# Optimization experiments

Hardware: AMD Instinct MI355X
Metric: run time of the kernel (lower is better)

## Reference

```python
import jax, jax.numpy as jnp
import numpy as np

L, D, H, F = 6, 1024, 8, 2048
B, S, IN = 4, 2048, 128
DK = D // H
EPS = 1e-6


def layer_norm(x, s, b):
    mu = jnp.mean(x, -1, keepdims=True)
    var = jnp.mean((x - mu) ** 2, -1, keepdims=True)
    return (x - mu) * jax.lax.rsqrt(var + EPS) * s + b


def rotate_every_two(x):
    x1 = x[..., ::2]
    x2 = x[..., 1::2]
    return jnp.stack([-x2, x1], axis=-1).reshape(x.shape)


def rotary_tables():
    # torchscale RetNet xpos-style angles: each freq repeated twice (interleaved)
    angle = 1.0 / (10000.0 ** jnp.linspace(0.0, 1.0, DK // 2))
    angle = jnp.repeat(angle, 2)                      # [DK]
    idx = jnp.arange(S, dtype=jnp.float32)[:, None]   # [S,1]
    return jnp.sin(idx * angle), jnp.cos(idx * angle)  # [S,DK] each


def decay_mask():
    # gamma_h = 1 - 2^(-5-h); D[h,n,m] = gamma_h^(n-m) for n>=m else 0,
    # row-normalized by sqrt(row sum) as in torchscale.
    gamma = 1.0 - 2.0 ** (-5.0 - jnp.arange(H, dtype=jnp.float32))  # [H]
    n = jnp.arange(S)
    diff = jnp.clip(n[:, None] - n[None, :], 0)                      # [S,S]
    tril = n[:, None] >= n[None, :]
    m = jnp.where(tril[None], gamma[:, None, None] ** diff[None].astype(jnp.float32), 0.0)
    return m / jnp.sqrt(jnp.sum(m, -1, keepdims=True))               # [H,S,S]


def setup_inputs() -> dict:
    key = jax.random.key(0)
    ks = iter(jax.random.split(key, 24))
    p = lambda shape: jax.random.normal(next(ks), shape, jnp.float32) * 0.02
    return {
        "x": jax.random.normal(next(ks), (B, S, IN), jnp.float32),
        "W_in": p((IN, D)), "b_in": jnp.zeros((D,), jnp.float32),
        "Wq": p((L, D, D)), "Wk": p((L, D, D)), "Wv": p((L, D, D)),
        "Wg": p((L, D, D)), "Wo": p((L, D, D)),
        "gn_g": jnp.ones((L, D), jnp.float32),
        "ln1_s": jnp.ones((L, D), jnp.float32), "ln1_b": jnp.zeros((L, D), jnp.float32),
        "ffn_W1": p((L, D, F)), "ffn_b1": jnp.zeros((L, F), jnp.float32),
        "ffn_W2": p((L, F, D)), "ffn_b2": jnp.zeros((L, D), jnp.float32),
        "ln2_s": jnp.ones((L, D), jnp.float32), "ln2_b": jnp.zeros((L, D), jnp.float32),
        "lnf_s": jnp.ones((D,), jnp.float32), "lnf_b": jnp.zeros((D,), jnp.float32),
        "W_reg": p((D, 1)), "b_reg": jnp.zeros((1,), jnp.float32),
    }


def reference(x, W_in, b_in, Wq, Wk, Wv, Wg, Wo, gn_g, ln1_s, ln1_b,
              ffn_W1, ffn_b1, ffn_W2, ffn_b2, ln2_s, ln2_b, lnf_s, lnf_b,
              W_reg, b_reg):
    sin, cos = rotary_tables()
    dmask = decay_mask()  # [H,S,S]
    h = x @ W_in + b_in   # input_embed
    for l in range(L):
        # --- multi-scale retention (pre-norm) ---
        y = layer_norm(h, ln1_s[l], ln1_b[l])
        q = (y @ Wq[l]).reshape(B, S, H, DK).transpose(0, 2, 1, 3)
        k = (y @ Wk[l]).reshape(B, S, H, DK).transpose(0, 2, 1, 3) * (DK ** -0.5)
        v = (y @ Wv[l]).reshape(B, S, H, DK).transpose(0, 2, 1, 3)
        q = q * cos + rotate_every_two(q) * sin
        k = k * cos + rotate_every_two(k) * sin
        scores = jnp.einsum('bhnd,bhmd->bhnm', q, k)
        ret = scores * dmask[None]
        ret = ret / jnp.clip(jnp.abs(ret).sum(-1, keepdims=True), 1.0, None)
        o = jnp.einsum('bhnm,bhmd->bhnd', ret, v)
        # per-head group (RMS) norm
        o = o * jax.lax.rsqrt(jnp.mean(o * o, -1, keepdims=True) + EPS)
        o = o.transpose(0, 2, 1, 3).reshape(B, S, D) * gn_g[l]
        g = y @ Wg[l]
        h = h + (jax.nn.silu(g) * o) @ Wo[l]
        # --- FFN (pre-norm) ---
        y = layer_norm(h, ln2_s[l], ln2_b[l])
        h = h + jax.nn.gelu(y @ ffn_W1[l] + ffn_b1[l]) @ ffn_W2[l] + ffn_b2[l]
    h = layer_norm(h, lnf_s, lnf_b)
    out = 1.1 * jax.nn.sigmoid(h @ W_reg + b_reg) - 0.05
    return out.squeeze(-1)  # [B,S]
```

## Files before the change

kernel.cpp:

```cpp
#include <hip/hip_runtime.h>

#define L_ 6
#define D_ 1024
#define H_ 8
#define F_ 2048
#define B_ 4
#define S_ 2048
#define IN_ 128
#define DK_ 128
#define BS_ (B_*S_)
#define D2_ 4096

typedef short bf16x8 __attribute__((ext_vector_type(8)));
typedef float f32x4 __attribute__((ext_vector_type(4)));

__device__ inline float b2f(unsigned short u){ union{unsigned int i; float f;} v; v.i = ((unsigned int)u)<<16; return v.f; }
__device__ inline unsigned short f2b(float f){ union{unsigned int i; float f;} v; v.f = f; unsigned int r = v.i + 0x7FFFu + ((v.i>>16)&1u); return (unsigned short)(r>>16); }
__device__ inline unsigned int cvtpk(float lo, float hi){
    unsigned int r; asm("v_cvt_pk_bf16_f32 %0, %1, %2" : "=v"(r) : "v"(lo), "v"(hi)); return r;
}

__device__ inline void gld16(const void* g, void* l) {
    __builtin_amdgcn_global_load_lds((const __attribute__((address_space(1))) unsigned int*)g,
                                     (__attribute__((address_space(3))) unsigned int*)l, 16, 0, 0);
}

#define GBAR() do{ asm volatile("" ::: "memory"); __builtin_amdgcn_s_barrier(); asm volatile("" ::: "memory"); }while(0)

__global__ void f32_to_bf16_k(const float* __restrict__ in, unsigned short* __restrict__ out, int n)
{
    int i = blockIdx.x*256 + threadIdx.x;
    if (i < n) out[i] = f2b(in[i]);
}

__global__ void transpose_w_k(const float* __restrict__ in, unsigned short* __restrict__ out, int R, int C, size_t ostride)
{
    __shared__ float tile[32][33];
    int z = blockIdx.z;
    const float* pi = in + (size_t)z*R*C;
    unsigned short* po = out + (size_t)z*ostride;
    int c0 = blockIdx.x*32, r0 = blockIdx.y*32;
    int tx = threadIdx.x, ty = threadIdx.y;
    #pragma unroll
    for (int i=0;i<4;i++) tile[ty+i*8][tx] = pi[(size_t)(r0+ty+i*8)*C + c0+tx];
    __syncthreads();
    #pragma unroll
    for (int i=0;i<4;i++) po[(size_t)(c0+ty+i*8)*R + r0+tx] = f2b(tile[tx][ty+i*8]);
}

__global__ void transpose_v_k(const unsigned short* __restrict__ vb, unsigned short* __restrict__ vT)
{
    __shared__ unsigned short tile[32][33];
    int z = blockIdx.z;
    int b = z >> 3, hh = z & 7;
    int s0 = blockIdx.x*32, d0 = blockIdx.y*32;
    int tx = threadIdx.x, ty = threadIdx.y;
    #pragma unroll
    for (int i=0;i<4;i++) tile[ty+i*8][tx] = vb[(size_t)(b*S_ + s0+ty+i*8)*D2_ + hh*DK_ + d0+tx];
    __syncthreads();
    #pragma unroll
    for (int i=0;i<4;i++) vT[((size_t)z*DK_ + d0+ty+i*8)*S_ + s0+tx] = tile[tx][ty+i*8];
}

__global__ void build_sincos_k(float* __restrict__ cost, float* __restrict__ sint)
{
    int id = blockIdx.x*256 + threadIdx.x;
    int s = id >> 6, i = id & 63;
    float ang = powf(10000.f, -(float)i/63.f);
    float a = (float)s * ang;
    float sv = sinf(a), cv = cosf(a);
    sint[s*DK_ + 2*i] = sv; sint[s*DK_ + 2*i+1] = sv;
    cost[s*DK_ + 2*i] = cv; cost[s*DK_ + 2*i+1] = cv;
}

__global__ void build_dnorm_k(float* __restrict__ dnorm)
{
    int id = blockIdx.x*256 + threadIdx.x;
    int h = id >> 11, n = id & (S_-1);
    double g = 1.0 - exp2((double)(-5 - h));
    double sum = (1.0 - exp(((double)(n+1))*log(g))) / (1.0 - g);
    dnorm[id] = (float)(1.0/sqrt(sum));
}

__device__ inline float bsum(float v, float* red, int t)
{
    #pragma unroll
    for (int m=32; m; m>>=1) v += __shfl_xor(v, m);
    __syncthreads();
    if ((t & 63) == 0) red[t>>6] = v;
    __syncthreads();
    return red[0]+red[1]+red[2]+red[3];
}

__global__ __launch_bounds__(256) void ln_to_bf16_k(const float* __restrict__ x, const float* __restrict__ s,
                                                    const float* __restrict__ b, unsigned short* __restrict__ y)
{
    __shared__ float red[4];
    int row = blockIdx.x, t = threadIdx.x;
    const float* xr = x + (size_t)row * D_;
    float4 v = ((const float4*)xr)[t];
    float mu = bsum(v.x+v.y+v.z+v.w, red, t) * (1.f/D_);
    float d0=v.x-mu, d1=v.y-mu, d2=v.z-mu, d3=v.w-mu;
    float var = bsum(d0*d0+d1*d1+d2*d2+d3*d3, red, t) * (1.f/D_);
    float inv = rsqrtf(var + 1e-6f);
    int c = t*4;
    float o0 = d0*inv*s[c+0] + b[c+0];
    float o1 = d1*inv*s[c+1] + b[c+1];
    float o2 = d2*inv*s[c+2] + b[c+2];
    float o3 = d3*inv*s[c+3] + b[c+3];
    unsigned long long pk = (unsigned long long)f2b(o0) | ((unsigned long long)f2b(o1)<<16)
                          | ((unsigned long long)f2b(o2)<<32) | ((unsigned long long)f2b(o3)<<48);
    *(unsigned long long*)(y + (size_t)row*D_ + c) = pk;
}

template<int MODE, int BM>
__global__ __launch_bounds__(512, (BM == 256) ? 2 : 4)
void gemm5(const unsigned short* __restrict__ A,
           const unsigned short* __restrict__ Bt,
           const float* __restrict__ bias,
           void* __restrict__ Cv,
           int M, int N, int K)
{
    constexpr int BN  = 256;
    constexpr int IR  = BM/2/16;
    constexpr int JR  = 4;
    constexpr int ASZ = BM*64;
    constexpr int BSZ = BN*64;
    constexpr int AP  = BM/128;
    constexpr int BP  = 2;
    constexpr int Sa  = AP + BP;
    __shared__ unsigned char lds[3*(ASZ+BSZ)];

    const int tid = threadIdx.x, lane = tid & 63, w = tid >> 6;
    const int r16 = lane & 15, quad = (lane >> 4) & 3;
    const int wm = w >> 2, wn = w & 3;

    const int nwg = (int)(gridDim.x * gridDim.y);
    int bid = (int)(blockIdx.y * gridDim.x + blockIdx.x);
    if ((nwg & 7) == 0) bid = (bid & 7) * (nwg >> 3) + (bid >> 3);
    const int m0 = (bid / (int)gridDim.x) * BM;
    const int n0 = (bid % (int)gridDim.x) * BN;

    const int srow = tid >> 2;
    const int schk = (tid & 3) ^ ((tid >> 3) & 3);
    const unsigned short* gA = A  + (size_t)(m0 + srow) * K + schk*8;
    const unsigned short* gB = Bt + (size_t)(n0 + srow) * K + schk*8;

    const int rchk = (quad ^ ((r16 >> 1) & 3)) * 16;
    const int aoff = (wm*(BM/2) + r16)*64 + rchk;
    const int boff = (wn*64 + r16)*64 + rchk;

    f32x4 acc[IR][JR];
    #pragma unroll
    for (int i=0;i<IR;i++)
      #pragma unroll
      for (int j=0;j<JR;j++) acc[i][j] = (f32x4){0.f,0.f,0.f,0.f};

    const int NT = K >> 5;

    auto stageA = [&](int t, int slot){
        unsigned char* la = lds + slot*(ASZ+BSZ);
        const size_t ko = (size_t)t * 32;
        #pragma unroll
        for (int p=0;p<AP;p++)
            gld16(gA + ko + (size_t)(p*128)*K, la + p*8192 + tid*16);
    };
    auto stageB = [&](int t, int slot){
        unsigned char* lb = lds + slot*(ASZ+BSZ) + ASZ;
        const size_t ko = (size_t)t * 32;
        #pragma unroll
        for (int p=0;p<BP;p++)
            gld16(gB + ko + (size_t)(p*128)*K, lb + p*8192 + tid*16);
    };

    stageA(0, 0); stageB(0, 0);
    stageA(1, 1); stageB(1, 1);
    if constexpr (Sa == 4) asm volatile("s_waitcnt vmcnt(4)" ::: "memory");
    else                   asm volatile("s_waitcnt vmcnt(3)" ::: "memory");
    GBAR();

    int st = 0;
    for (int t = 0; t < NT; ++t) {
        const unsigned char* ab = lds + st*(ASZ+BSZ);
        const unsigned char* bb = ab + ASZ;
        int s2 = st + 2; if (s2 >= 3) s2 -= 3;
        const bool pre = (t + 2 < NT);

        bf16x8 af[IR], bg[JR];
        #pragma unroll
        for (int i=0;i<IR/2;i++) af[i] = *(const bf16x8*)(ab + aoff + i*1024);
        #pragma unroll
        for (int j=0;j<JR;j++)   bg[j] = *(const bf16x8*)(bb + boff + j*1024);
        if (pre) stageA(t+2, s2);
        GBAR();
        asm volatile("s_waitcnt lgkmcnt(0)" ::: "memory");
        __builtin_amdgcn_s_setprio(1);
        #pragma unroll
        for (int i=0;i<IR/2;i++)
          #pragma unroll
          for (int j=0;j<JR;j++)
            acc[i][j] = __builtin_amdgcn_mfma_f32_16x16x32_bf16(af[i], bg[j], acc[i][j], 0,0,0);
        __builtin_amdgcn_s_setprio(0);
        GBAR();

        #pragma unroll
        for (int i=IR/2;i<IR;i++) af[i] = *(const bf16x8*)(ab + aoff + i*1024);
        if (pre) {
            stageB(t+2, s2);
            if constexpr (Sa == 4) asm volatile("s_waitcnt vmcnt(4)" ::: "memory");
            else                   asm volatile("s_waitcnt vmcnt(3)" ::: "memory");
        } else if (t + 1 < NT) {
            asm volatile("s_waitcnt vmcnt(0)" ::: "memory");
        }
        GBAR();
        asm volatile("s_waitcnt lgkmcnt(0)" ::: "memory");
        __builtin_amdgcn_s_setprio(1);
        #pragma unroll
        for (int i=IR/2;i<IR;i++)
          #pragma unroll
          for (int j=0;j<JR;j++)
            acc[i][j] = __builtin_amdgcn_mfma_f32_16x16x32_bf16(af[i], bg[j], acc[i][j], 0,0,0);
        __builtin_amdgcn_s_setprio(0);
        GBAR();

        st = (st + 1 == 3) ? 0 : st + 1;
    }

    float* Cf = (float*)Cv;
    unsigned short* Cb = (unsigned short*)Cv;
    #pragma unroll
    for (int j=0;j<JR;j++) {
      const int ccol = n0 + wn*64 + j*16 + r16;
      const float bv = bias ? bias[ccol] : 0.f;
      #pragma unroll
      for (int i=0;i<IR;i++) {
        #pragma unroll
        for (int r=0;r<4;r++) {
          const int crow = m0 + wm*(BM/2) + i*16 + quad*4 + r;
          float v = acc[i][j][r];
          if (MODE == 0) { Cf[(size_t)crow*N + ccol] = v + bv; }
          else if (MODE == 1) { Cf[(size_t)crow*N + ccol] += v + bv; }
          else if (MODE == 2) { Cb[(size_t)crow*N + ccol] = f2b(v); }
          else {
            v += bv;
            float t3 = tanhf(0.7978845608028654f*(v + 0.044715f*v*v*v));
            Cb[(size_t)crow*N + ccol] = f2b(0.5f*v*(1.f + t3));
          }
        }
      }
    }
}

__global__ __launch_bounds__(256) void rope_qk_k(unsigned short* __restrict__ qkvg,
                                                 const float* __restrict__ cost, const float* __restrict__ sint)
{
    int id = blockIdx.x*256 + threadIdx.x;
    int row = id >> 9;
    int d = (id & 511) * 2;
    int s = row & (S_-1);
    int dk = d & (DK_-1);
    float c0 = cost[s*DK_ + dk],   s0 = sint[s*DK_ + dk];
    float c1 = cost[s*DK_ + dk+1], s1 = sint[s*DK_ + dk+1];
    size_t off = (size_t)row*D2_ + d;
    unsigned int qu = *(unsigned int*)(qkvg + off);
    float q0 = b2f((unsigned short)(qu & 0xffffu)), q1 = b2f((unsigned short)(qu >> 16));
    float r0 = q0*c0 - q1*s0;
    float r1 = q1*c1 + q0*s1;
    *(unsigned int*)(qkvg + off) = (unsigned int)f2b(r0) | ((unsigned int)f2b(r1) << 16);
    const float sc = 0.08838834764831845f;
    unsigned int ku = *(unsigned int*)(qkvg + off + 1024);
    float k0 = b2f((unsigned short)(ku & 0xffffu))*sc, k1 = b2f((unsigned short)(ku >> 16))*sc;
    float t0 = k0*c0 - k1*s0;
    float t1 = k1*c1 + k0*s1;
    *(unsigned int*)(qkvg + off + 1024) = (unsigned int)f2b(t0) | ((unsigned int)f2b(t1) << 16);
}

__global__ __launch_bounds__(256, 2) void retention_k(const unsigned short* __restrict__ qk_base,
    const unsigned short* __restrict__ vT, const float* __restrict__ dnorm,
    const float* __restrict__ gng, unsigned short* __restrict__ attnin)
{
    __shared__ __align__(16) unsigned char lds[75776];
    const int pr = blockIdx.x;
    const int bh = blockIdx.y;
    const int b = bh >> 3, hh = bh & 7;
    const int tid = threadIdx.x, lane = tid & 63, w = tid >> 6;
    const int r16 = lane & 15, quad = lane >> 4;

    const float l2g = log2f(1.f - exp2f(-5.f - (float)hh));
    const int ithr = (int)(45.f / (-l2g));
    const unsigned int mkr = (r16 & 7) << 4;

    const int mk2  = ((tid >> 4) & 7) << 4;
    const int mkv2 = ((tid >> 3) & 7) << 4;
    const unsigned short* ksrc = qk_base + 1024 + ((size_t)(b*S_) + (tid>>4))*D2_ + hh*DK_
                                + ((((tid&15)*16) ^ mk2) >> 1);
    const unsigned short* vsrc = vT + ((size_t)bh*DK_ + (tid>>3))*S_ + ((((tid&7)*16) ^ mkv2) >> 1);

    float Aarr[4];
    #pragma unroll
    for (int r=0;r<4;r++) Aarr[r] = exp2f(l2g * (float)(63 - (w*16 + quad*4 + r)));

    float* dsums = (float*)(lds + 73728);
    float* ssums = (float*)(lds + 74752);

    auto stage = [&](int c2, int kt2){
        const unsigned short* s0 = ksrc + (size_t)kt2*64*D2_;
        #pragma unroll
        for (int i=0;i<4;i++)
            gld16(s0 + (size_t)i*16*D2_, lds + c2*16384 + i*4096 + w*1024);
        const unsigned short* s1 = vsrc + kt2*64;
        #pragma unroll
        for (int j=0;j<4;j++)
            gld16(s1 + (size_t)j*32*S_, lds + 32768 + c2*16384 + j*4096 + w*1024);
    };

    int cur = 0;

    #pragma unroll 1
    for (int seg = 0; seg < 2; ++seg) {
        const int qt = seg ? pr : (31 - pr);
        const int n0 = qt * 64;
        const int kt_start = max(0, (n0 - ithr) >> 6);

        bf16x8 qf[4][4];
        const unsigned short* qptr = qk_base + ((size_t)(b*S_ + n0 + r16))*D2_ + hh*DK_;
        #pragma unroll
        for (int qtl=0;qtl<4;qtl++)
          #pragma unroll
          for (int c=0;c<4;c++) qf[qtl][c] = *(const bf16x8*)(qptr + qtl*16*D2_ + c*32 + quad*8);

        f32x4 oacc[4][2];
        #pragma unroll
        for (int qtl=0;qtl<4;qtl++)
          #pragma unroll
          for (int dt=0;dt<2;dt++) oacc[qtl][dt] = (f32x4){0.f,0.f,0.f,0.f};
        float dsum[4] = {0.f,0.f,0.f,0.f};

        stage(cur, kt_start);

        #pragma unroll 1
        for (int kt = kt_start; kt <= qt; ++kt) {
            if (kt < qt) { stage(cur^1, kt+1); asm volatile("s_waitcnt vmcnt(8)" ::: "memory"); }
            else         { asm volatile("s_waitcnt vmcnt(0)" ::: "memory"); }
            GBAR();

            const unsigned char* kb = lds + cur*16384;
            bf16x8 kf[4];
            #pragma unroll
            for (int c=0;c<4;c++)
                kf[c] = *(const bf16x8*)(kb + (w*16 + r16)*256 + ((c*64 + quad*16) ^ mkr));
            f32x4 sf[4];
            #pragma unroll
            for (int qtl=0;qtl<4;qtl++) sf[qtl] = (f32x4){0.f,0.f,0.f,0.f};
            __builtin_amdgcn_s_setprio(1);
            #pragma unroll
            for (int c=0;c<4;c++)
              #pragma unroll
              for (int qtl=0;qtl<4;qtl++)
                sf[qtl] = __builtin_amdgcn_mfma_f32_16x16x32_bf16(kf[c], qf[qtl][c], sf[qtl], 0,0,0);
            __builtin_amdgcn_s_setprio(0);

            const bool diag = (kt == qt);
            #pragma unroll
            for (int qtl=0;qtl<4;qtl++) {
                float Bq = exp2f(l2g * (float)(n0 + qtl*16 + r16 - kt*64 - 63));
                float pv[4];
                #pragma unroll
                for (int r=0;r<4;r++) {
                    float p = sf[qtl][r] * Aarr[r] * Bq;
                    if (diag && (w*16 + quad*4 + r > qtl*16 + r16)) p = 0.f;
                    dsum[qtl] += fabsf(p);
                    pv[r] = p;
                }
                unsigned long long pk = (unsigned long long)cvtpk(pv[0], pv[1])
                                      | ((unsigned long long)cvtpk(pv[2], pv[3]) << 32);
                *(unsigned long long*)(lds + 65536 + (qtl*16 + r16)*128 + ((w*32 + quad*8) ^ mkr)) = pk;
            }
            asm volatile("s_waitcnt lgkmcnt(0)" ::: "memory");
            GBAR();

            const unsigned char* vb = lds + 32768 + cur*16384;
            bf16x8 pa[4][2], vf[2][2];
            #pragma unroll
            for (int qtl=0;qtl<4;qtl++)
              #pragma unroll
              for (int ks=0;ks<2;ks++)
                pa[qtl][ks] = *(const bf16x8*)(lds + 65536 + (qtl*16 + r16)*128 + ((ks*64 + quad*16) ^ mkr));
            #pragma unroll
            for (int dt=0;dt<2;dt++)
              #pragma unroll
              for (int ks=0;ks<2;ks++)
                vf[dt][ks] = *(const bf16x8*)(vb + (w*32 + dt*16 + r16)*128 + ((ks*64 + quad*16) ^ mkr));
            __builtin_amdgcn_s_setprio(1);
            #pragma unroll
            for (int qtl=0;qtl<4;qtl++)
              #pragma unroll
              for (int dt=0;dt<2;dt++)
                #pragma unroll
                for (int ks=0;ks<2;ks++)
                  oacc[qtl][dt] = __builtin_amdgcn_mfma_f32_16x16x32_bf16(pa[qtl][ks], vf[dt][ks], oacc[qtl][dt], 0,0,0);
            __builtin_amdgcn_s_setprio(0);
            GBAR();
            cur ^= 1;
        }

        #pragma unroll
        for (int qtl=0;qtl<4;qtl++) {
            float dv = dsum[qtl];
            dv += __shfl_xor(dv, 16); dv += __shfl_xor(dv, 32);
            if (lane < 16) dsums[w*64 + qtl*16 + r16] = dv;
        }
        __syncthreads();
        float scl[4][4], pss[4][4];
        #pragma unroll
        for (int qtl=0;qtl<4;qtl++) {
            #pragma unroll
            for (int r=0;r<4;r++) {
                int nl = qtl*16 + quad*4 + r;
                float dv = dsums[nl] + dsums[64+nl] + dsums[128+nl] + dsums[192+nl];
                float nr = dnorm[hh*S_ + n0 + nl];
                float sc = nr / fmaxf(1.f, dv * nr);
                scl[qtl][r] = sc;
                float s2 = 0.f;
                #pragma unroll
                for (int dt=0;dt<2;dt++) { float t = oacc[qtl][dt][r]*sc; s2 += t*t; }
                s2 += __shfl_xor(s2,1); s2 += __shfl_xor(s2,2);
                s2 += __shfl_xor(s2,4); s2 += __shfl_xor(s2,8);
                pss[qtl][r] = s2;
            }
        }
        if (r16 == 0) {
            #pragma unroll
            for (int qtl=0;qtl<4;qtl++)
              #pragma unroll
              for (int r=0;r<4;r++)
                ssums[w*64 + qtl*16 + quad*4 + r] = pss[qtl][r];
        }
        __syncthreads();
        #pragma unroll
        for (int qtl=0;qtl<4;qtl++) {
            float rms[4];
            #pragma unroll
            for (int r=0;r<4;r++) {
                int nl = qtl*16 + quad*4 + r;
                float s2 = ssums[nl] + ssums[64+nl] + ssums[128+nl] + ssums[192+nl];
                rms[r] = rsqrtf(s2*(1.f/DK_) + 1e-6f);
            }
            #pragma unroll
            for (int dt=0;dt<2;dt++) {
                int d = w*32 + dt*16 + r16;
                float gg = gng[hh*DK_ + d];
                #pragma unroll
                for (int r=0;r<4;r++) {
                    int n = n0 + qtl*16 + quad*4 + r;
                    float gv = b2f(qk_base[(size_t)(b*S_ + n)*D2_ + 3072 + hh*DK_ + d]);
                    float sg = gv / (1.f + expf(-gv));
                    float ov = oacc[qtl][dt][r]*scl[qtl][r]*rms[r]*gg;
                    attnin[(size_t)(b*S_ + n)*D_ + hh*DK_ + d] = f2b(ov*sg);
                }
            }
        }
        __syncthreads();
    }
}

__global__ __launch_bounds__(256) void head_out_k(const float* __restrict__ h, const float* __restrict__ s,
    const float* __restrict__ b, const float* __restrict__ wreg, const float* __restrict__ breg,
    float* __restrict__ out)
{
    __shared__ float red[4];
    int row = blockIdx.x, t = threadIdx.x;
    const float* xr = h + (size_t)row*D_;
    float4 v = ((const float4*)xr)[t];
    float mu = bsum(v.x+v.y+v.z+v.w, red, t) * (1.f/D_);
    float d0=v.x-mu, d1=v.y-mu, d2=v.z-mu, d3=v.w-mu;
    float var = bsum(d0*d0+d1*d1+d2*d2+d3*d3, red, t) * (1.f/D_);
    float inv = rsqrtf(var + 1e-6f);
    int c = t*4;
    float dot = (d0*inv*s[c+0]+b[c+0])*wreg[c+0] + (d1*inv*s[c+1]+b[c+1])*wreg[c+1]
              + (d2*inv*s[c+2]+b[c+2])*wreg[c+2] + (d3*inv*s[c+3]+b[c+3])*wreg[c+3];
    dot = bsum(dot, red, t);
    if (t == 0) out[row] = 1.1f / (1.f + expf(-(dot + breg[0]))) - 0.05f;
}

extern "C" void kernel_launch(void* const* d_in, const int* in_sizes, int n_in,
                              void* d_out, int out_size, void* d_ws, size_t ws_size,
                              hipStream_t stream)
{
    (void)in_sizes; (void)n_in; (void)out_size; (void)ws_size;
    const float* x    = (const float*)d_in[0];
    const float* W_in = (const float*)d_in[1];
    const float* b_in = (const float*)d_in[2];
    const float* Wq   = (const float*)d_in[3];
    const float* Wk   = (const float*)d_in[4];
    const float* Wv   = (const float*)d_in[5];
    const float* Wg   = (const float*)d_in[6];
    const float* Wo   = (const float*)d_in[7];
    const float* gn_g = (const float*)d_in[8];
    const float* ln1s = (const float*)d_in[9];
    const float* ln1b = (const float*)d_in[10];
    const float* W1   = (const float*)d_in[11];
    const float* b1   = (const float*)d_in[12];
    const float* W2   = (const float*)d_in[13];
    const float* b2   = (const float*)d_in[14];
    const float* ln2s = (const float*)d_in[15];
    const float* ln2b = (const float*)d_in[16];
    const float* lnfs = (const float*)d_in[17];
    const float* lnfb = (const float*)d_in[18];
    const float* Wreg = (const float*)d_in[19];
    const float* breg = (const float*)d_in[20];

    char* ws = (char*)d_ws;
    size_t off = 0;
    auto alloc = [&](size_t bytes) { char* p = ws + off; off += (bytes + 255) & ~(size_t)255; return p; };

    const size_t DD = (size_t)D_*D_;
    unsigned short* wqkvgT = (unsigned short*)alloc((size_t)L_*4*DD*2);
    unsigned short* woT  = (unsigned short*)alloc((size_t)L_*DD*2);
    unsigned short* w1T  = (unsigned short*)alloc((size_t)L_*D_*F_*2);
    unsigned short* w2T  = (unsigned short*)alloc((size_t)L_*D_*F_*2);
    unsigned short* winT = (unsigned short*)alloc((size_t)D_*IN_*2);
    unsigned short* x_bf = (unsigned short*)alloc((size_t)BS_*IN_*2);
    float*          hbuf = (float*)alloc((size_t)BS_*D_*4);
    unsigned short* y_bf = (unsigned short*)alloc((size_t)BS_*D_*2);
    unsigned short* qkvg = (unsigned short*)alloc((size_t)BS_*D2_*2);
    unsigned short* vTb  = (unsigned short*)alloc((size_t)BS_*D_*2);
    float*          cost = (float*)alloc((size_t)S_*DK_*4);
    float*          sint = (float*)alloc((size_t)S_*DK_*4);
    float*          dnrm = (float*)alloc((size_t)H_*S_*4);
    unsigned short* attn = y_bf;
    unsigned short* midb = qkvg;

    dim3 tb(32, 8);

    f32_to_bf16_k<<<(BS_*IN_)/256, 256, 0, stream>>>(x, x_bf, BS_*IN_);
    transpose_w_k<<<dim3(32,32,L_), tb, 0, stream>>>(Wq, wqkvgT + 0*DD, D_, D_, 4*DD);
    transpose_w_k<<<dim3(32,32,L_), tb, 0, stream>>>(Wk, wqkvgT + 1*DD, D_, D_, 4*DD);
    transpose_w_k<<<dim3(32,32,L_), tb, 0, stream>>>(Wv, wqkvgT + 2*DD, D_, D_, 4*DD);
    transpose_w_k<<<dim3(32,32,L_), tb, 0, stream>>>(Wg, wqkvgT + 3*DD, D_, D_, 4*DD);
    transpose_w_k<<<dim3(32,32,L_), tb, 0, stream>>>(Wo, woT, D_, D_, DD);
    transpose_w_k<<<dim3(64,32,L_), tb, 0, stream>>>(W1, w1T, D_, F_, (size_t)D_*F_);
    transpose_w_k<<<dim3(32,64,L_), tb, 0, stream>>>(W2, w2T, F_, D_, (size_t)D_*F_);
    transpose_w_k<<<dim3(32, 4, 1), tb, 0, stream>>>(W_in, winT, IN_, D_, (size_t)D_*IN_);
    build_sincos_k<<<(S_*64)/256, 256, 0, stream>>>(cost, sint);
    build_dnorm_k<<<(H_*S_)/256, 256, 0, stream>>>(dnrm);

    gemm5<0,128><<<dim3(D_/256, BS_/128), 512, 0, stream>>>(x_bf, winT, b_in, hbuf, BS_, D_, IN_);

    for (int l = 0; l < L_; ++l) {
        ln_to_bf16_k<<<BS_, 256, 0, stream>>>(hbuf, ln1s + l*D_, ln1b + l*D_, y_bf);
        gemm5<2,256><<<dim3(D2_/256, BS_/256), 512, 0, stream>>>(y_bf, wqkvgT + (size_t)l*4*DD, nullptr, qkvg, BS_, D2_, D_);
        rope_qk_k<<<(BS_*D_/2)/256, 256, 0, stream>>>(qkvg, cost, sint);
        transpose_v_k<<<dim3(S_/32, DK_/32, B_*H_), tb, 0, stream>>>(qkvg + 2048, vTb);
        retention_k<<<dim3(16, B_*H_), 256, 0, stream>>>(qkvg, vTb, dnrm, gn_g + l*D_, attn);
        gemm5<1,128><<<dim3(D_/256, BS_/128), 512, 0, stream>>>(attn, woT + (size_t)l*DD, nullptr, hbuf, BS_, D_, D_);
        ln_to_bf16_k<<<BS_, 256, 0, stream>>>(hbuf, ln2s + l*D_, ln2b + l*D_, y_bf);
        gemm5<3,256><<<dim3(F_/256, BS_/256), 512, 0, stream>>>(y_bf, w1T + (size_t)l*D_*F_, b1 + l*F_, midb, BS_, F_, D_);
        gemm5<1,128><<<dim3(D_/256, BS_/128), 512, 0, stream>>>(midb, w2T + (size_t)l*D_*F_, b2 + l*D_, hbuf, BS_, D_, F_);
    }

    head_out_k<<<BS_, 256, 0, stream>>>(hbuf, lnfs, lnfb, Wreg, breg, (float*)d_out);
}
```

Measured before the change: 2.132 ms.

## Rework GEMM to double-buffered 64-wide K tiles with BM fixed at 256

The GEMM kernel moves from a three-slot ring of 32-wide K tiles to a two-buffer scheme where each stage holds a 64-wide K step split into two 32-wide sub-tiles. BM is fixed at 256 and BN is now the template parameter, so the narrow-output GEMMs use 256x128 tiles instead of 128x256. The aim is to halve the outer-loop iterations and barrier overhead per K element while keeping prefetch of the next stage overlapped with MFMA work. In exchange, LDS use per block grows and the wait counts and barrier placement become more delicate.

```diff
diff --git a/kernel.cpp b/kernel.cpp
--- a/kernel.cpp
+++ b/kernel.cpp
@@ -113,23 +113,23 @@
     *(unsigned long long*)(y + (size_t)row*D_ + c) = pk;
 }
 
-template<int MODE, int BM>
-__global__ __launch_bounds__(512, (BM == 256) ? 2 : 4)
-void gemm5(const unsigned short* __restrict__ A,
+template<int MODE, int BN>
+__global__ __launch_bounds__(512, 2)
+void gemm6(const unsigned short* __restrict__ A,
            const unsigned short* __restrict__ Bt,
            const float* __restrict__ bias,
            void* __restrict__ Cv,
            int M, int N, int K)
 {
-    constexpr int BN  = 256;
-    constexpr int IR  = BM/2/16;
-    constexpr int JR  = 4;
-    constexpr int ASZ = BM*64;
-    constexpr int BSZ = BN*64;
-    constexpr int AP  = BM/128;
-    constexpr int BP  = 2;
-    constexpr int Sa  = AP + BP;
-    __shared__ unsigned char lds[3*(ASZ+BSZ)];
+    constexpr int BM   = 256;
+    constexpr int IR   = 8;
+    constexpr int JR   = BN/64;
+    constexpr int ASUB = BM*64;
+    constexpr int BSUB = BN*64;
+    constexpr int BUFSZ= 2*ASUB + 2*BSUB;
+    constexpr int AP   = 2;
+    constexpr int BP   = BN/128;
+    __shared__ unsigned char lds[2*BUFSZ];
 
     const int tid = threadIdx.x, lane = tid & 63, w = tid >> 6;
     const int r16 = lane & 15, quad = (lane >> 4) & 3;
@@ -147,8 +147,8 @@
     const unsigned short* gB = Bt + (size_t)(n0 + srow) * K + schk*8;
 
     const int rchk = (quad ^ ((r16 >> 1) & 3)) * 16;
-    const int aoff = (wm*(BM/2) + r16)*64 + rchk;
-    const int boff = (wn*64 + r16)*64 + rchk;
+    const int aoff = (wm*128 + r16)*64 + rchk;
+    const int boff = (wn*(BN/4) + r16)*64 + rchk;
 
     f32x4 acc[IR][JR];
     #pragma unroll
@@ -156,95 +156,111 @@
       #pragma unroll
       for (int j=0;j<JR;j++) acc[i][j] = (f32x4){0.f,0.f,0.f,0.f};
 
-    const int NT = K >> 5;
-
-    auto stageA = [&](int t, int slot){
-        unsigned char* la = lds + slot*(ASZ+BSZ);
-        const size_t ko = (size_t)t * 32;
+    const int NT = K >> 6;
+
+    auto stageA = [&](int t, int kk){
+        unsigned char* dst = lds + (t&1)*BUFSZ + kk*ASUB;
+        const unsigned short* src = gA + (size_t)t*64 + kk*32;
         #pragma unroll
         for (int p=0;p<AP;p++)
-            gld16(gA + ko + (size_t)(p*128)*K, la + p*8192 + tid*16);
+            gld16(src + (size_t)(p*128)*K, dst + p*8192 + tid*16);
     };
-    auto stageB = [&](int t, int slot){
-        unsigned char* lb = lds + slot*(ASZ+BSZ) + ASZ;
-        const size_t ko = (size_t)t * 32;
+    auto stageB = [&](int t, int kk){
+        unsigned char* dst = lds + (t&1)*BUFSZ + 2*ASUB + kk*BSUB;
+        const unsigned short* src = gB + (size_t)t*64 + kk*32;
         #pragma unroll
         for (int p=0;p<BP;p++)
-            gld16(gB + ko + (size_t)(p*128)*K, lb + p*8192 + tid*16);
+            gld16(src + (size_t)(p*128)*K, dst + p*8192 + tid*16);
     };
 
-    stageA(0, 0); stageB(0, 0);
-    stageA(1, 1); stageB(1, 1);
-    if constexpr (Sa == 4) asm volatile("s_waitcnt vmcnt(4)" ::: "memory");
+    stageA(0,0); stageB(0,0); stageA(0,1); stageB(0,1);
+    if constexpr (BN==256) asm volatile("s_waitcnt vmcnt(4)" ::: "memory");
     else                   asm volatile("s_waitcnt vmcnt(3)" ::: "memory");
     GBAR();
 
-    int st = 0;
     for (int t = 0; t < NT; ++t) {
-        const unsigned char* ab = lds + st*(ASZ+BSZ);
-        const unsigned char* bb = ab + ASZ;
-        int s2 = st + 2; if (s2 >= 3) s2 -= 3;
-        const bool pre = (t + 2 < NT);
-
-        bf16x8 af[IR], bg[JR];
-        #pragma unroll
-        for (int i=0;i<IR/2;i++) af[i] = *(const bf16x8*)(ab + aoff + i*1024);
-        #pragma unroll
-        for (int j=0;j<JR;j++)   bg[j] = *(const bf16x8*)(bb + boff + j*1024);
-        if (pre) stageA(t+2, s2);
-        GBAR();
-        asm volatile("s_waitcnt lgkmcnt(0)" ::: "memory");
-        __builtin_amdgcn_s_setprio(1);
-        #pragma unroll
-        for (int i=0;i<IR/2;i++)
-          #pragma unroll
-          for (int j=0;j<JR;j++)
-            acc[i][j] = __builtin_amdgcn_mfma_f32_16x16x32_bf16(af[i], bg[j], acc[i][j], 0,0,0);
-        __builtin_amdgcn_s_setprio(0);
-        GBAR();
-
-        #pragma unroll
-        for (int i=IR/2;i<IR;i++) af[i] = *(const bf16x8*)(ab + aoff + i*1024);
-        if (pre) {
-            stageB(t+2, s2);
-            if constexpr (Sa == 4) asm volatile("s_waitcnt vmcnt(4)" ::: "memory");
-            else                   asm volatile("s_waitcnt vmcnt(3)" ::: "memory");
-        } else if (t + 1 < NT) {
-            asm volatile("s_waitcnt vmcnt(0)" ::: "memory");
-        }
-        GBAR();
-        asm volatile("s_waitcnt lgkmcnt(0)" ::: "memory");
-        __builtin_amdgcn_s_setprio(1);
-        #pragma unroll
-        for (int i=IR/2;i<IR;i++)
-          #pragma unroll
-          for (int j=0;j<JR;j++)
-            acc[i][j] = __builtin_amdgcn_mfma_f32_16x16x32_bf16(af[i], bg[j], acc[i][j], 0,0,0);
-        __builtin_amdgcn_s_setprio(0);
-        GBAR();
-
-        st = (st + 1 == 3) ? 0 : st + 1;
+        const unsigned char* cb = lds + (t&1)*BUFSZ;
+        const bool pre = (t+1 < NT);
+        #pragma unroll
+        for (int kk = 0; kk < 2; ++kk) {
+            const unsigned char* ak = cb + kk*ASUB;
+            const unsigned char* bk = cb + 2*ASUB + kk*BSUB;
+            if constexpr (BN == 256) {
+                bf16x8 af[4], bg[JR];
+                #pragma unroll
+                for (int i=0;i<4;i++) af[i] = *(const bf16x8*)(ak + aoff + i*1024);
+                #pragma unroll
+                for (int j=0;j<JR;j++) bg[j] = *(const bf16x8*)(bk + boff + j*1024);
+                if (pre) stageA(t+1, kk);
+                GBAR();
+                asm volatile("s_waitcnt lgkmcnt(0)" ::: "memory");
+                __builtin_amdgcn_s_setprio(1);
+                #pragma unroll
+                for (int i=0;i<4;i++)
+                  #pragma unroll
+                  for (int j=0;j<JR;j++)
+                    acc[i][j] = __builtin_amdgcn_mfma_f32_16x16x32_bf16(af[i], bg[j], acc[i][j], 0,0,0);
+                __builtin_amdgcn_s_setprio(0);
+                GBAR();
+                #pragma unroll
+                for (int i=0;i<4;i++) af[i] = *(const bf16x8*)(ak + aoff + (4+i)*1024);
+                if (pre) stageB(t+1, kk);
+                GBAR();
+                asm volatile("s_waitcnt lgkmcnt(0)" ::: "memory");
+                __builtin_amdgcn_s_setprio(1);
+                #pragma unroll
+                for (int i=0;i<4;i++)
+                  #pragma unroll
+                  for (int j=0;j<JR;j++)
+                    acc[4+i][j] = __builtin_amdgcn_mfma_f32_16x16x32_bf16(af[i], bg[j], acc[4+i][j], 0,0,0);
+                __builtin_amdgcn_s_setprio(0);
+                if (pre) asm volatile("s_waitcnt vmcnt(4)" ::: "memory");
+                else     asm volatile("s_waitcnt vmcnt(0)" ::: "memory");
+                GBAR();
+            } else {
+                bf16x8 af[8], bg[JR];
+                #pragma unroll
+                for (int i=0;i<8;i++) af[i] = *(const bf16x8*)(ak + aoff + i*1024);
+                #pragma unroll
+                for (int j=0;j<JR;j++) bg[j] = *(const bf16x8*)(bk + boff + j*1024);
+                if (pre) { stageA(t+1, kk); stageB(t+1, kk); }
+                GBAR();
+                asm volatile("s_waitcnt lgkmcnt(0)" ::: "memory");
+                __builtin_amdgcn_s_setprio(1);
+                #pragma unroll
+                for (int i=0;i<8;i++)
+                  #pragma unroll
+                  for (int j=0;j<JR;j++)
+                    acc[i][j] = __builtin_amdgcn_mfma_f32_16x16x32_bf16(af[i], bg[j], acc[i][j], 0,0,0);
+                __builtin_amdgcn_s_setprio(0);
+                if (pre) asm volatile("s_waitcnt vmcnt(3)" ::: "memory");
+                else     asm volatile("s_waitcnt vmcnt(0)" ::: "memory");
+                GBAR();
+            }
+        }
     }
 
     float* Cf = (float*)Cv;
     unsigned short* Cb = (unsigned short*)Cv;
-    #pragma unroll
-    for (int j=0;j<JR;j++) {
-      const int ccol = n0 + wn*64 + j*16 + r16;
-      const float bv = bias ? bias[ccol] : 0.f;
+    float bvs[JR];
+    #pragma unroll
+    for (int j=0;j<JR;j++) bvs[j] = bias ? bias[n0 + wn*(BN/4) + j*16 + r16] : 0.f;
+    #pragma unroll
+    for (int i=0;i<IR;i++) {
       #pragma unroll
-      for (int i=0;i<IR;i++) {
-        #pragma unroll
-        for (int r=0;r<4;r++) {
-          const int crow = m0 + wm*(BM/2) + i*16 + quad*4 + r;
+      for (int r=0;r<4;r++) {
+        const size_t crow = (size_t)(m0 + wm*128 + i*16 + quad*4 + r);
+        #pragma unroll
+        for (int j=0;j<JR;j++) {
+          const int ccol = n0 + wn*(BN/4) + j*16 + r16;
           float v = acc[i][j][r];
-          if (MODE == 0) { Cf[(size_t)crow*N + ccol] = v + bv; }
-          else if (MODE == 1) { Cf[(size_t)crow*N + ccol] += v + bv; }
-          else if (MODE == 2) { Cb[(size_t)crow*N + ccol] = f2b(v); }
+          if (MODE == 0) { Cf[crow*N + ccol] = v + bvs[j]; }
+          else if (MODE == 1) { Cf[crow*N + ccol] += v + bvs[j]; }
+          else if (MODE == 2) { Cb[crow*N + ccol] = f2b(v); }
           else {
-            v += bv;
+            v += bvs[j];
             float t3 = tanhf(0.7978845608028654f*(v + 0.044715f*v*v*v));
-            Cb[(size_t)crow*N + ccol] = f2b(0.5f*v*(1.f + t3));
+            Cb[crow*N + ccol] = f2b(0.5f*v*(1.f + t3));
           }
         }
       }
@@ -545,18 +561,18 @@
     build_sincos_k<<<(S_*64)/256, 256, 0, stream>>>(cost, sint);
     build_dnorm_k<<<(H_*S_)/256, 256, 0, stream>>>(dnrm);
 
-    gemm5<0,128><<<dim3(D_/256, BS_/128), 512, 0, stream>>>(x_bf, winT, b_in, hbuf, BS_, D_, IN_);
+    gemm6<0,128><<<dim3(D_/128, BS_/256), 512, 0, stream>>>(x_bf, winT, b_in, hbuf, BS_, D_, IN_);
 
     for (int l = 0; l < L_; ++l) {
         ln_to_bf16_k<<<BS_, 256, 0, stream>>>(hbuf, ln1s + l*D_, ln1b + l*D_, y_bf);
-        gemm5<2,256><<<dim3(D2_/256, BS_/256), 512, 0, stream>>>(y_bf, wqkvgT + (size_t)l*4*DD, nullptr, qkvg, BS_, D2_, D_);
+        gemm6<2,256><<<dim3(D2_/256, BS_/256), 512, 0, stream>>>(y_bf, wqkvgT + (size_t)l*4*DD, nullptr, qkvg, BS_, D2_, D_);
         rope_qk_k<<<(BS_*D_/2)/256, 256, 0, stream>>>(qkvg, cost, sint);
         transpose_v_k<<<dim3(S_/32, DK_/32, B_*H_), tb, 0, stream>>>(qkvg + 2048, vTb);
         retention_k<<<dim3(16, B_*H_), 256, 0, stream>>>(qkvg, vTb, dnrm, gn_g + l*D_, attn);
-        gemm5<1,128><<<dim3(D_/256, BS_/128), 512, 0, stream>>>(attn, woT + (size_t)l*DD, nullptr, hbuf, BS_, D_, D_);
+        gemm6<1,128><<<dim3(D_/128, BS_/256), 512, 0, stream>>>(attn, woT + (size_t)l*DD, nullptr, hbuf, BS_, D_, D_);
         ln_to_bf16_k<<<BS_, 256, 0, stream>>>(hbuf, ln2s + l*D_, ln2b + l*D_, y_bf);
-        gemm5<3,256><<<dim3(F_/256, BS_/256), 512, 0, stream>>>(y_bf, w1T + (size_t)l*D_*F_, b1 + l*F_, midb, BS_, F_, D_);
-        gemm5<1,128><<<dim3(D_/256, BS_/128), 512, 0, stream>>>(midb, w2T + (size_t)l*D_*F_, b2 + l*D_, hbuf, BS_, D_, F_);
+        gemm6<3,256><<<dim3(F_/256, BS_/256), 512, 0, stream>>>(y_bf, w1T + (size_t)l*D_*F_, b1 + l*F_, midb, BS_, F_, D_);
+        gemm6<1,128><<<dim3(D_/128, BS_/256), 512, 0, stream>>>(midb, w2T + (size_t)l*D_*F_, b2 + l*D_, hbuf, BS_, D_, F_);
     }
 
     head_out_k<<<BS_, 256, 0, stream>>>(hbuf, lnfs, lnfb, Wreg, breg, (float*)d_out);
```

Result: faster. 2.022 ms (-5.2%).
